# Kernel optimization log

Measured on AMD Instinct MI355X. Metric: run time of the kernel, lower is better.

Reference implementation:

```python
import jax, jax.numpy as jnp
import numpy as np
from jax import lax

N_CLASSES = 10
N_EXPERTS = 45  # 10 choose 2
EPS = 1e-5

# lookup table: (i1, i2) with i1 < i2 -> flat expert id (matches nested loop order)
_tbl = np.zeros((N_CLASSES, N_CLASSES), dtype=np.int32)
_k = 0
for _i1 in range(N_CLASSES):
    for _i2 in range(_i1 + 1, N_CLASSES):
        _tbl[_i1, _i2] = _k
        _k += 1
PAIR_TABLE = jnp.asarray(_tbl)


def _downscale(x):
    # AvgPool2d(3, stride=3) on 28x28 -> 9x9 (floor: uses top-left 27x27)
    B = x.shape[0]
    return x[:, :, :27, :27].reshape(B, 1, 9, 3, 9, 3).mean(axis=(3, 5))


def _bn_eval(h, gamma, beta, mean, var):
    scale = gamma * lax.rsqrt(var + EPS)
    return h * scale[None, :, None, None] + (beta - mean * scale)[None, :, None, None]


def _stage1(x, w1, b1, g1, be1, m1, v1, fcw1, fcb1):
    xd = _downscale(x)                                         # [B,1,9,9]
    h = lax.conv_general_dilated(xd, w1, (1, 1), 'VALID',
                                 dimension_numbers=('NCHW', 'OIHW', 'NCHW'))
    h = h + b1[None, :, None, None]                            # [B,20,7,7]
    h = _bn_eval(h, g1, be1, m1, v1)
    h = jax.nn.relu(h)
    B = h.shape[0]
    h = h[:, :, :6, :6].reshape(B, 20, 3, 2, 3, 2).max(axis=(3, 5))  # maxpool2 -> [B,20,3,3]
    h = h.reshape(B, 180)
    return h @ fcw1.T + fcb1                                   # [B,10] raw logits


def reference(x, w1, b1, g1, be1, m1, v1, fcw1, fcb1,
              w2, b2, g2, be2, m2, v2, fcw2, fcb2):
    B = x.shape[0]
    logits1 = _stage1(x, w1, b1, g1, be1, m1, v1, fcw1, fcb1)  # [B,10]
    ls1 = jax.nn.log_softmax(logits1, axis=1)

    # routing: top-2 class indices, sorted ascending, -> pairwise expert id
    top2 = jnp.sort(jnp.argsort(ls1, axis=1)[:, -2:], axis=1)  # [B,2]
    idx0, idx1 = top2[:, 0], top2[:, 1]
    eid = PAIR_TABLE[idx0, idx1]                               # [B]

    # stage 2 (TinyNet2) with per-example gathered expert params
    xd = _downscale(x)                                         # [B,1,9,9]
    # extract 5x5 conv patches (valid, stride 1): output spatial 5x5
    patches = jnp.stack([xd[:, 0, i:i + 5, j:j + 5]
                         for i in range(5) for j in range(5)], axis=1)  # [B,25,5,5]
    Wsel = w2.reshape(N_EXPERTS, 15, 25)[eid]                  # [B,15,25]
    h = jnp.einsum('bkhw,bok->bohw', patches, Wsel) + b2[eid][:, :, None, None]  # [B,15,5,5]
    scale = (g2 * lax.rsqrt(v2 + EPS))[eid]                    # [B,15]
    shift = (be2 - m2 * g2 * lax.rsqrt(v2 + EPS))[eid]
    h = h * scale[:, :, None, None] + shift[:, :, None, None]
    h = jax.nn.relu(h)
    h = h[:, :, :4, :4].reshape(B, 15, 2, 2, 2, 2).max(axis=(3, 5))  # [B,15,2,2]
    feat = h.reshape(B, 60)
    s2 = jnp.einsum('bf,bof->bo', feat, fcw2[eid]) + fcb2[eid]  # [B,2]

    # combine: scatter the two expert logits into the routed columns
    rows = jnp.arange(B)
    out = jnp.full((B, N_CLASSES), -100.0, dtype=logits1.dtype)
    out = out.at[rows, idx0].set(s2[:, 0]).at[rows, idx1].set(s2[:, 1])
    # eval-mode bypass: use stage1 raw logits if max log-prob > 0.3
    use1 = jnp.max(ls1, axis=1) > 0.3
    out = jnp.where(use1[:, None], logits1, out)
    out = jax.nn.log_softmax(out, axis=1)
    return (logits1, out)


def setup_inputs() -> dict:
    key = jax.random.key(0)
    ks = jax.random.split(key, 18)
    B = 65536
    s = 0.1
    return {
        'x': jax.random.normal(ks[0], (B, 1, 28, 28), dtype=jnp.float32),
        # stage1 (TinyNet, 20 kernels, k=3)
        'w1': jax.random.normal(ks[1], (20, 1, 3, 3), dtype=jnp.float32) * s,
        'b1': jax.random.normal(ks[2], (20,), dtype=jnp.float32) * s,
        'g1': jax.random.normal(ks[3], (20,), dtype=jnp.float32) * s + 1.0,
        'be1': jax.random.normal(ks[4], (20,), dtype=jnp.float32) * s,
        'm1': jax.random.normal(ks[5], (20,), dtype=jnp.float32) * s,
        'v1': jax.random.uniform(ks[6], (20,), dtype=jnp.float32) + 0.5,
        'fcw1': jax.random.normal(ks[7], (10, 180), dtype=jnp.float32) * s,
        'fcb1': jax.random.normal(ks[8], (10,), dtype=jnp.float32) * s,
        # 45 stacked stage2 experts (TinyNet2, 15 kernels, k=5)
        'w2': jax.random.normal(ks[9], (45, 15, 1, 5, 5), dtype=jnp.float32) * s,
        'b2': jax.random.normal(ks[10], (45, 15), dtype=jnp.float32) * s,
        'g2': jax.random.normal(ks[11], (45, 15), dtype=jnp.float32) * s + 1.0,
        'be2': jax.random.normal(ks[12], (45, 15), dtype=jnp.float32) * s,
        'm2': jax.random.normal(ks[13], (45, 15), dtype=jnp.float32) * s,
        'v2': jax.random.uniform(ks[14], (45, 15), dtype=jnp.float32) + 0.5,
        'fcw2': jax.random.normal(ks[15], (45, 2, 60), dtype=jnp.float32) * s,
        'fcb2': jax.random.normal(ks[16], (45, 2), dtype=jnp.float32) * s,
    }
```

## Files before the change

### kernel.cpp

```cpp
#include <hip/hip_runtime.h>
#include <cmath>

#define EPSF 1e-5f

#define OFF_FC2   19576
#define OFF_IMG   25088

#define I_W1P    0
#define I_FCW1R  240
#define I_B1F    2400
#define I_FCB1   2420
#define I_B2F    2432
#define I_FCB2   3108

__global__ __launch_bounds__(256) void setup_tables(
    const float* __restrict__ w1, const float* __restrict__ b1,
    const float* __restrict__ g1, const float* __restrict__ be1,
    const float* __restrict__ m1, const float* __restrict__ v1,
    const float* __restrict__ w2, const float* __restrict__ b2,
    const float* __restrict__ g2, const float* __restrict__ be2,
    const float* __restrict__ m2, const float* __restrict__ v2,
    const float* __restrict__ fcw2, const float* __restrict__ fcb2,
    const float* __restrict__ fcw1, const float* __restrict__ fcb1,
    float* __restrict__ ws)
{
  const int t  = blockIdx.x * blockDim.x + threadIdx.x;
  const int nt = gridDim.x * blockDim.x;
  float* W2F  = ws;
  float* FC2P = ws + OFF_FC2;
  float* IMG  = ws + OFF_IMG;

  for (int idx = t; idx < 18900; idx += nt) {
    int kk = idx & 3, rest = idx >> 2;
    int e = rest % 45, ok4 = rest / 45;
    int k4 = ok4 % 7, o = ok4 / 7;
    int k = k4 * 4 + kk;
    float s = g2[e*15+o] / sqrtf(v2[e*15+o] + EPSF);
    W2F[idx] = (k < 25) ? w2[(e*15+o)*25 + k] * s : 0.0f;
  }
  for (int idx = t; idx < 5400; idx += nt) {
    int e = idx % 45, r = idx / 45;
    int pos = r % 4, r2 = r / 4;
    int o = r2 % 15, oo = r2 / 15;
    FC2P[idx] = fcw2[(e*2+oo)*60 + o*4 + pos];
  }
  for (int i = t; i < 4096; i += nt) {
    float v = 0.0f;
    if (i < I_FCW1R) {
      int ch = i / 12, j = i % 12;
      if (j < 9) {
        float s = g1[ch] / sqrtf(v1[ch] + EPSF);
        v = w1[ch*9 + j] * s;
      }
    } else if (i < I_B1F) {
      int k = i - I_FCW1R;
      int c = k % 12, r2 = k / 12, pp = r2 % 9, ch = r2 / 9;
      if (c < 10) v = fcw1[c*180 + ch*9 + pp];
    } else if (i < I_FCB1) {
      int ch = i - I_B1F;
      float s = g1[ch] / sqrtf(v1[ch] + EPSF);
      v = b1[ch]*s + be1[ch] - m1[ch]*s;
    } else if (i < I_B2F) {
      int k = i - I_FCB1;
      if (k < 10) v = fcb1[k];
    } else if (i < I_FCB2) {
      int k = i - I_B2F;
      if (k < 675) {
        int e = k % 45, o = k / 45;
        float s = g2[e*15+o] / sqrtf(v2[e*15+o] + EPSF);
        v = b2[e*15+o]*s + be2[e*15+o] - m2[e*15+o]*s;
      }
    } else {
      int k = i - I_FCB2;
      if (k < 90) {
        int e = k % 45, oo = k / 45;
        v = fcb2[e*2+oo];
      }
    }
    IMG[i] = v;
  }
}

#define GETC(arr, k) ((k)%4==0 ? arr[(k)/4].x : (k)%4==1 ? arr[(k)/4].y : \
                      (k)%4==2 ? arr[(k)/4].z : arr[(k)/4].w)

#define T_RAW   4352
#define T_TAB   4352
#define SSTR    676

__global__ __launch_bounds__(256) void fused_k(
    const float* __restrict__ x,
    const float* __restrict__ ws,
    float* __restrict__ out, int B)
{
  __shared__ float lds[9760];

  const int t  = threadIdx.x;
  const int p  = t & 3;
  const int sl = t >> 2;
  const int b  = blockIdx.x * 64 + sl;
  const bool valid = (b < B);

  const int s8  = t >> 5;
  const int tin = t & 31;

  float4 pre[6];
  {
    const int bs = blockIdx.x * 64 + s8;
    if (bs < B) {
      const float4* xp = reinterpret_cast<const float4*>(x + (size_t)bs * 784);
      #pragma unroll
      for (int j = 0; j < 5; j++) pre[j] = xp[tin + 32*j];
      pre[5] = (tin < 8) ? xp[tin + 160] : make_float4(0.f,0.f,0.f,0.f);
    } else {
      #pragma unroll
      for (int j = 0; j < 6; j++) pre[j] = make_float4(0.f,0.f,0.f,0.f);
    }
    float4* rw = reinterpret_cast<float4*>(&lds[T_RAW + s8*SSTR]);
    #pragma unroll
    for (int j = 0; j < 5; j++) rw[tin + 32*j] = pre[j];
    if (tin < 8) rw[tin + 160] = pre[5];
  }
  __syncthreads();

  #pragma unroll 1
  for (int c = 0; c < 8; c++) {
    if (c < 7) {
      const int bs = blockIdx.x * 64 + (c+1)*8 + s8;
      if (bs < B) {
        const float4* xp = reinterpret_cast<const float4*>(x + (size_t)bs * 784);
        #pragma unroll
        for (int j = 0; j < 5; j++) pre[j] = xp[tin + 32*j];
        pre[5] = (tin < 8) ? xp[tin + 160] : make_float4(0.f,0.f,0.f,0.f);
      }
    }
    if (t < 128) {
      const int ds8  = t >> 4;
      const int orow = (t >> 1) & 7;
      const int h    = t & 1;
      float a0 = 0.f, a1 = 0.f, a2 = 0.f, a3 = 0.f;
      #pragma unroll
      for (int dr = 0; dr < 3; dr++) {
        const float4* rp = reinterpret_cast<const float4*>(
            &lds[T_RAW + ds8*SSTR + (3*orow + dr)*28 + 12*h]);
        float4 q0 = rp[0], q1 = rp[1], q2 = rp[2];
        a0 += q0.x + q0.y + q0.z;
        a1 += q0.w + q1.x + q1.y;
        a2 += q1.z + q1.w + q2.x;
        a3 += q2.y + q2.z + q2.w;
      }
      float4* dst = reinterpret_cast<float4*>(&lds[(c*8 + ds8)*68 + orow*8 + 4*h]);
      *dst = make_float4(a0*(1.f/9.f), a1*(1.f/9.f), a2*(1.f/9.f), a3*(1.f/9.f));
    }
    __syncthreads();
    if (c < 7) {
      float4* rw = reinterpret_cast<float4*>(&lds[T_RAW + s8*SSTR]);
      #pragma unroll
      for (int j = 0; j < 5; j++) rw[tin + 32*j] = pre[j];
      if (tin < 8) rw[tin + 160] = pre[5];
      __syncthreads();
    }
  }

  const float4* img4 = reinterpret_cast<const float4*>(ws + OFF_IMG);
  float4 tv0 = img4[t];
  float4 tv1 = img4[t + 256];
  float4 tv2 = img4[t + 512];
  float4 tv3 = img4[t + 768];

  const int R0 = p & 2;
  const int C0 = (p & 1) * 2;
  float xl[36];
  #pragma unroll
  for (int lr = 0; lr < 6; lr++) {
    const float2* src = reinterpret_cast<const float2*>(&lds[sl*68 + (R0+lr)*8 + C0]);
    float2 q0 = src[0], q1 = src[1], q2 = src[2];
    xl[lr*6+0]=q0.x; xl[lr*6+1]=q0.y; xl[lr*6+2]=q1.x;
    xl[lr*6+3]=q1.y; xl[lr*6+4]=q2.x; xl[lr*6+5]=q2.y;
  }
  {
    float4* tab4 = reinterpret_cast<float4*>(&lds[T_TAB]);
    tab4[t] = tv0; tab4[t + 256] = tv1; tab4[t + 512] = tv2; tab4[t + 768] = tv3;
  }
  __syncthreads();

  const int basegpp = (p >> 1) * 3 + (p & 1);
  float logits[10];
  #pragma unroll
  for (int c = 0; c < 10; c++) logits[c] = 0.0f;

  #pragma unroll 1
  for (int ch = 0; ch < 20; ch++) {
    const float4* wp = reinterpret_cast<const float4*>(&lds[T_TAB + I_W1P + ch*12]);
    float4 w0 = wp[0], w1v = wp[1], w2v = wp[2];
    const float w_[9] = {w0.x,w0.y,w0.z,w0.w,w1v.x,w1v.y,w1v.z,w1v.w,w2v.x};
    const float bb = lds[T_TAB + I_B1F + ch];
    #pragma unroll
    for (int lp = 0; lp < 4; lp++) {
      const int lpr = lp >> 1, lpc = lp & 1;
      float c00 = bb, c01 = bb, c10 = bb, c11 = bb;
      #pragma unroll
      for (int dr = 0; dr < 3; dr++) {
        #pragma unroll
        for (int dc = 0; dc < 3; dc++) {
          const float wk = w_[dr*3 + dc];
          c00 = fmaf(xl[(2*lpr+0+dr)*6 + 2*lpc+0+dc], wk, c00);
          c01 = fmaf(xl[(2*lpr+0+dr)*6 + 2*lpc+1+dc], wk, c01);
          c10 = fmaf(xl[(2*lpr+1+dr)*6 + 2*lpc+0+dc], wk, c10);
          c11 = fmaf(xl[(2*lpr+1+dr)*6 + 2*lpc+1+dc], wk, c11);
        }
      }
      float f = fmaxf(fmaxf(fmaxf(c00, c01), fmaxf(c10, c11)), 0.0f);
      const int MASKS[4] = {3, 14, 5, 12};
      const float fm = ((MASKS[lp] >> p) & 1) ? f : 0.0f;
      const int off = (lp >> 1) * 3 + (lp & 1);
      const float4* f4 = reinterpret_cast<const float4*>(
          &lds[T_TAB + I_FCW1R + (ch*9 + basegpp + off)*12]);
      float4 f0 = f4[0], f1 = f4[1], f2 = f4[2];
      logits[0] = fmaf(fm, f0.x, logits[0]);
      logits[1] = fmaf(fm, f0.y, logits[1]);
      logits[2] = fmaf(fm, f0.z, logits[2]);
      logits[3] = fmaf(fm, f0.w, logits[3]);
      logits[4] = fmaf(fm, f1.x, logits[4]);
      logits[5] = fmaf(fm, f1.y, logits[5]);
      logits[6] = fmaf(fm, f1.z, logits[6]);
      logits[7] = fmaf(fm, f1.w, logits[7]);
      logits[8] = fmaf(fm, f2.x, logits[8]);
      logits[9] = fmaf(fm, f2.y, logits[9]);
    }
  }

  #pragma unroll
  for (int c = 0; c < 10; c++) {
    float v = logits[c];
    v += __shfl_xor(v, 1);
    v += __shfl_xor(v, 2);
    logits[c] = v + lds[T_TAB + I_FCB1 + c];
  }

  int i1 = 0; float v1m = logits[0];
  #pragma unroll
  for (int c = 1; c < 10; c++) { if (logits[c] >= v1m) { v1m = logits[c]; i1 = c; } }
  int i2 = 0; float v2m = -3.0e38f;
  #pragma unroll
  for (int c = 0; c < 10; c++) { if (c != i1 && logits[c] >= v2m) { v2m = logits[c]; i2 = c; } }
  const int idx0 = i1 < i2 ? i1 : i2;
  const int idx1 = i1 < i2 ? i2 : i1;
  int eid = 8*idx0 - (idx0*(idx0-1))/2 + idx1 - 1;
  eid = eid < 0 ? 0 : (eid > 44 ? 44 : eid);

  float sume = 0.0f;
  #pragma unroll
  for (int c = 0; c < 10; c++) sume += __expf(logits[c] - v1m);
  const bool use1 = (-__logf(sume)) > 0.3f;

  __syncthreads();
  if (p == 0) {
    #pragma unroll
    for (int c = 0; c < 5; c++) lds[sl*10 + c] = logits[c];
  } else if (p == 1) {
    #pragma unroll
    for (int c = 5; c < 10; c++) lds[sl*10 + c] = logits[c];
  }

  const float4* W2F4 = reinterpret_cast<const float4*>(ws);
  const float*  FC2P = ws + OFF_FC2;
  float s2a = 0.0f, s2b = 0.0f;

  #pragma unroll 1
  for (int o = 0; o < 15; o++) {
    float4 wv[7];
    #pragma unroll
    for (int k4 = 0; k4 < 7; k4++) wv[k4] = W2F4[(o*7 + k4)*45 + eid];
    const float bias = lds[T_TAB + I_B2F + o*45 + eid];
    const float fa = FC2P[(o*4 + p)*45 + eid];
    const float fb = FC2P[((15 + o)*4 + p)*45 + eid];
    float c00 = bias, c01 = bias, c10 = bias, c11 = bias;
    #pragma unroll
    for (int i = 0; i < 5; i++) {
      #pragma unroll
      for (int j = 0; j < 5; j++) {
        const float wk = GETC(wv, i*5 + j);
        c00 = fmaf(xl[(0+i)*6 + 0+j], wk, c00);
        c01 = fmaf(xl[(0+i)*6 + 1+j], wk, c01);
        c10 = fmaf(xl[(1+i)*6 + 0+j], wk, c10);
        c11 = fmaf(xl[(1+i)*6 + 1+j], wk, c11);
      }
    }
    const float f = fmaxf(fmaxf(fmaxf(c00, c01), fmaxf(c10, c11)), 0.0f);
    s2a = fmaf(f, fa, s2a);
    s2b = fmaf(f, fb, s2b);
  }
  s2a += __shfl_xor(s2a, 1); s2a += __shfl_xor(s2a, 2);
  s2b += __shfl_xor(s2b, 1); s2b += __shfl_xor(s2b, 2);
  s2a += lds[T_TAB + I_FCB2 + eid];
  s2b += lds[T_TAB + I_FCB2 + 45 + eid];

  __syncthreads();
  float o10[10];
  #pragma unroll
  for (int c = 0; c < 10; c++) {
    float v = -100.0f;
    v = (c == idx0) ? s2a : v;
    v = (c == idx1) ? s2b : v;
    o10[c] = use1 ? lds[sl*10 + c] : v;
  }
  float m2x = o10[0];
  #pragma unroll
  for (int c = 1; c < 10; c++) m2x = fmaxf(m2x, o10[c]);
  float se2 = 0.0f;
  #pragma unroll
  for (int c = 0; c < 10; c++) se2 += __expf(o10[c] - m2x);
  const float lse2 = m2x + __logf(se2);

  if (p == 2) {
    #pragma unroll
    for (int c = 0; c < 5; c++) lds[640 + sl*10 + c] = o10[c] - lse2;
  } else if (p == 3) {
    #pragma unroll
    for (int c = 5; c < 10; c++) lds[640 + sl*10 + c] = o10[c] - lse2;
  }
  __syncthreads();

  if (blockIdx.x * 64 + 64 <= B) {
    const float4* l4 = reinterpret_cast<const float4*>(lds);
    const size_t o1 = (size_t)blockIdx.x * 640;
    if (t < 160)
      *reinterpret_cast<float4*>(out + o1 + (size_t)t*4) = l4[t];
    if (t >= 96)
      *reinterpret_cast<float4*>(out + (size_t)B*10 + o1 + (size_t)(t-96)*4) = l4[160 + (t-96)];
  } else if (valid) {
    const size_t base = (size_t)b * 10;
    if (p == 0) {
      #pragma unroll
      for (int c = 0; c < 5; c++) out[base + c] = lds[sl*10 + c];
    } else if (p == 1) {
      #pragma unroll
      for (int c = 5; c < 10; c++) out[base + c] = lds[sl*10 + c];
    } else if (p == 2) {
      #pragma unroll
      for (int c = 0; c < 5; c++) out[(size_t)B*10 + base + c] = lds[640 + sl*10 + c];
    } else {
      #pragma unroll
      for (int c = 5; c < 10; c++) out[(size_t)B*10 + base + c] = lds[640 + sl*10 + c];
    }
  }
}

extern "C" void kernel_launch(void* const* d_in, const int* in_sizes, int n_in,
                              void* d_out, int out_size, void* d_ws, size_t ws_size,
                              hipStream_t stream) {
  const float* x    = (const float*)d_in[0];
  const float* w1   = (const float*)d_in[1];
  const float* b1   = (const float*)d_in[2];
  const float* g1   = (const float*)d_in[3];
  const float* be1  = (const float*)d_in[4];
  const float* m1   = (const float*)d_in[5];
  const float* v1   = (const float*)d_in[6];
  const float* fcw1 = (const float*)d_in[7];
  const float* fcb1 = (const float*)d_in[8];
  const float* w2   = (const float*)d_in[9];
  const float* b2   = (const float*)d_in[10];
  const float* g2   = (const float*)d_in[11];
  const float* be2  = (const float*)d_in[12];
  const float* m2   = (const float*)d_in[13];
  const float* v2   = (const float*)d_in[14];
  const float* fcw2 = (const float*)d_in[15];
  const float* fcb2 = (const float*)d_in[16];
  float* out = (float*)d_out;
  float* ws  = (float*)d_ws;
  const int B = in_sizes[0] / 784;

  setup_tables<<<80, 256, 0, stream>>>(w1, b1, g1, be1, m1, v1,
                                       w2, b2, g2, be2, m2, v2,
                                       fcw2, fcb2, fcw1, fcb1, ws);
  fused_k<<<(B + 63)/64, 256, 0, stream>>>(x, ws, out, B);
}
```

Before: 345.5 us.

## Read parameter tables from global memory instead of staging them in LDS

The fused kernel no longer copies a parameter table into shared memory. Stage-1 weights, biases and FC weights are now read directly from the global workspace, which drops a global-to-LDS staging pass and one barrier. The stage-2 bias and FC bias are packed into the padding slots of the per-expert weight vector, so they arrive with the weight load. The FC1 accumulation is restructured so each lane picks its own pooled feature per position. Every block now pays for scalar or cached global loads inside its inner loops and does more FMAs with zero operands.

After: 358.8 us. +3.8%, slower.

```diff
diff --git a/kernel.cpp b/kernel.cpp
--- a/kernel.cpp
+++ b/kernel.cpp
@@ -3,15 +3,10 @@
 
 #define EPSF 1e-5f
 
-#define OFF_FC2   19576
-#define OFF_IMG   25088
-
-#define I_W1P    0
-#define I_FCW1R  240
-#define I_B1F    2400
-#define I_FCB1   2420
-#define I_B2F    2432
-#define I_FCB2   3108
+#define OFF_FC2P  18900
+#define OFF_FCW1R 24300
+#define OFF_W1F   26460
+#define OFF_B1F   26640
 
 __global__ __launch_bounds__(256) void setup_tables(
     const float* __restrict__ w1, const float* __restrict__ b1,
@@ -21,14 +16,16 @@
     const float* __restrict__ g2, const float* __restrict__ be2,
     const float* __restrict__ m2, const float* __restrict__ v2,
     const float* __restrict__ fcw2, const float* __restrict__ fcb2,
-    const float* __restrict__ fcw1, const float* __restrict__ fcb1,
+    const float* __restrict__ fcw1,
     float* __restrict__ ws)
 {
   const int t  = blockIdx.x * blockDim.x + threadIdx.x;
   const int nt = gridDim.x * blockDim.x;
-  float* W2F  = ws;
-  float* FC2P = ws + OFF_FC2;
-  float* IMG  = ws + OFF_IMG;
+  float* W2F   = ws;
+  float* FC2P  = ws + OFF_FC2P;
+  float* FCW1R = ws + OFF_FCW1R;
+  float* W1F   = ws + OFF_W1F;
+  float* B1F   = ws + OFF_B1F;
 
   for (int idx = t; idx < 18900; idx += nt) {
     int kk = idx & 3, rest = idx >> 2;
@@ -36,7 +33,12 @@
     int k4 = ok4 % 7, o = ok4 / 7;
     int k = k4 * 4 + kk;
     float s = g2[e*15+o] / sqrtf(v2[e*15+o] + EPSF);
-    W2F[idx] = (k < 25) ? w2[(e*15+o)*25 + k] * s : 0.0f;
+    float v;
+    if (k < 25)       v = w2[(e*15+o)*25 + k] * s;
+    else if (k == 25) v = b2[e*15+o]*s + be2[e*15+o] - m2[e*15+o]*s;
+    else if (k == 26) v = (o == 0) ? fcb2[e*2 + 0] : 0.0f;
+    else              v = (o == 0) ? fcb2[e*2 + 1] : 0.0f;
+    W2F[idx] = v;
   }
   for (int idx = t; idx < 5400; idx += nt) {
     int e = idx % 45, r = idx / 45;
@@ -44,40 +46,18 @@
     int o = r2 % 15, oo = r2 / 15;
     FC2P[idx] = fcw2[(e*2+oo)*60 + o*4 + pos];
   }
-  for (int i = t; i < 4096; i += nt) {
-    float v = 0.0f;
-    if (i < I_FCW1R) {
-      int ch = i / 12, j = i % 12;
-      if (j < 9) {
-        float s = g1[ch] / sqrtf(v1[ch] + EPSF);
-        v = w1[ch*9 + j] * s;
-      }
-    } else if (i < I_B1F) {
-      int k = i - I_FCW1R;
-      int c = k % 12, r2 = k / 12, pp = r2 % 9, ch = r2 / 9;
-      if (c < 10) v = fcw1[c*180 + ch*9 + pp];
-    } else if (i < I_FCB1) {
-      int ch = i - I_B1F;
-      float s = g1[ch] / sqrtf(v1[ch] + EPSF);
-      v = b1[ch]*s + be1[ch] - m1[ch]*s;
-    } else if (i < I_B2F) {
-      int k = i - I_FCB1;
-      if (k < 10) v = fcb1[k];
-    } else if (i < I_FCB2) {
-      int k = i - I_B2F;
-      if (k < 675) {
-        int e = k % 45, o = k / 45;
-        float s = g2[e*15+o] / sqrtf(v2[e*15+o] + EPSF);
-        v = b2[e*15+o]*s + be2[e*15+o] - m2[e*15+o]*s;
-      }
-    } else {
-      int k = i - I_FCB2;
-      if (k < 90) {
-        int e = k % 45, oo = k / 45;
-        v = fcb2[e*2+oo];
-      }
-    }
-    IMG[i] = v;
+  for (int idx = t; idx < 2160; idx += nt) {
+    int c = idx % 12, r2 = idx / 12, pp = r2 % 9, ch = r2 / 9;
+    FCW1R[idx] = (c < 10) ? fcw1[c*180 + ch*9 + pp] : 0.0f;
+  }
+  for (int idx = t; idx < 180; idx += nt) {
+    int ch = idx / 9;
+    float s = g1[ch] / sqrtf(v1[ch] + EPSF);
+    W1F[idx] = w1[idx] * s;
+  }
+  for (int idx = t; idx < 20; idx += nt) {
+    float s = g1[idx] / sqrtf(v1[idx] + EPSF);
+    B1F[idx] = b1[idx]*s + be1[idx] - m1[idx]*s;
   }
 }
 
@@ -85,12 +65,12 @@
                       (k)%4==2 ? arr[(k)/4].z : arr[(k)/4].w)
 
 #define T_RAW   4352
-#define T_TAB   4352
 #define SSTR    676
 
 __global__ __launch_bounds__(256) void fused_k(
     const float* __restrict__ x,
     const float* __restrict__ ws,
+    const float* __restrict__ fcb1,
     float* __restrict__ out, int B)
 {
   __shared__ float lds[9760];
@@ -100,6 +80,11 @@
   const int sl = t >> 2;
   const int b  = blockIdx.x * 64 + sl;
   const bool valid = (b < B);
+
+  const float* FC2P  = ws + OFF_FC2P;
+  const float* FCW1R = ws + OFF_FCW1R;
+  const float* W1F   = ws + OFF_W1F;
+  const float* B1F   = ws + OFF_B1F;
 
   const int s8  = t >> 5;
   const int tin = t & 31;
@@ -162,12 +147,6 @@
     }
   }
 
-  const float4* img4 = reinterpret_cast<const float4*>(ws + OFF_IMG);
-  float4 tv0 = img4[t];
-  float4 tv1 = img4[t + 256];
-  float4 tv2 = img4[t + 512];
-  float4 tv3 = img4[t + 768];
-
   const int R0 = p & 2;
   const int C0 = (p & 1) * 2;
   float xl[36];
@@ -178,23 +157,18 @@
     xl[lr*6+0]=q0.x; xl[lr*6+1]=q0.y; xl[lr*6+2]=q1.x;
     xl[lr*6+3]=q1.y; xl[lr*6+4]=q2.x; xl[lr*6+5]=q2.y;
   }
-  {
-    float4* tab4 = reinterpret_cast<float4*>(&lds[T_TAB]);
-    tab4[t] = tv0; tab4[t + 256] = tv1; tab4[t + 512] = tv2; tab4[t + 768] = tv3;
-  }
-  __syncthreads();
-
-  const int basegpp = (p >> 1) * 3 + (p & 1);
+
   float logits[10];
   #pragma unroll
   for (int c = 0; c < 10; c++) logits[c] = 0.0f;
 
   #pragma unroll 1
   for (int ch = 0; ch < 20; ch++) {
-    const float4* wp = reinterpret_cast<const float4*>(&lds[T_TAB + I_W1P + ch*12]);
-    float4 w0 = wp[0], w1v = wp[1], w2v = wp[2];
-    const float w_[9] = {w0.x,w0.y,w0.z,w0.w,w1v.x,w1v.y,w1v.z,w1v.w,w2v.x};
-    const float bb = lds[T_TAB + I_B1F + ch];
+    float w_[9];
+    #pragma unroll
+    for (int k = 0; k < 9; k++) w_[k] = W1F[ch*9 + k];
+    const float bb = B1F[ch];
+    float feat[4];
     #pragma unroll
     for (int lp = 0; lp < 4; lp++) {
       const int lpr = lp >> 1, lpc = lp & 1;
@@ -210,23 +184,16 @@
           c11 = fmaf(xl[(2*lpr+1+dr)*6 + 2*lpc+1+dc], wk, c11);
         }
       }
-      float f = fmaxf(fmaxf(fmaxf(c00, c01), fmaxf(c10, c11)), 0.0f);
-      const int MASKS[4] = {3, 14, 5, 12};
-      const float fm = ((MASKS[lp] >> p) & 1) ? f : 0.0f;
-      const int off = (lp >> 1) * 3 + (lp & 1);
-      const float4* f4 = reinterpret_cast<const float4*>(
-          &lds[T_TAB + I_FCW1R + (ch*9 + basegpp + off)*12]);
-      float4 f0 = f4[0], f1 = f4[1], f2 = f4[2];
-      logits[0] = fmaf(fm, f0.x, logits[0]);
-      logits[1] = fmaf(fm, f0.y, logits[1]);
-      logits[2] = fmaf(fm, f0.z, logits[2]);
-      logits[3] = fmaf(fm, f0.w, logits[3]);
-      logits[4] = fmaf(fm, f1.x, logits[4]);
-      logits[5] = fmaf(fm, f1.y, logits[5]);
-      logits[6] = fmaf(fm, f1.z, logits[6]);
-      logits[7] = fmaf(fm, f1.w, logits[7]);
-      logits[8] = fmaf(fm, f2.x, logits[8]);
-      logits[9] = fmaf(fm, f2.y, logits[9]);
+      feat[lp] = fmaxf(fmaxf(fmaxf(c00, c01), fmaxf(c10, c11)), 0.0f);
+    }
+    const int QOWN[9]  = {0,1,1,0,2,3,2,2,3};
+    const int LPOWN[9] = {0,0,1,2,1,1,2,3,3};
+    #pragma unroll
+    for (int pp = 0; pp < 9; pp++) {
+      const float* R = FCW1R + (ch*9 + pp)*12;
+      const float fm = (p == QOWN[pp]) ? feat[LPOWN[pp]] : 0.0f;
+      #pragma unroll
+      for (int c = 0; c < 10; c++) logits[c] = fmaf(fm, R[c], logits[c]);
     }
   }
 
@@ -235,7 +202,7 @@
     float v = logits[c];
     v += __shfl_xor(v, 1);
     v += __shfl_xor(v, 2);
-    logits[c] = v + lds[T_TAB + I_FCB1 + c];
+    logits[c] = v + fcb1[c];
   }
 
   int i1 = 0; float v1m = logits[0];
@@ -264,37 +231,45 @@
   }
 
   const float4* W2F4 = reinterpret_cast<const float4*>(ws);
-  const float*  FC2P = ws + OFF_FC2;
-  float s2a = 0.0f, s2b = 0.0f;
+
+  const float4 wb = W2F4[6*45 + eid];
+  float s2a = (p == 0) ? wb.z : 0.0f;
+  float s2b = (p == 0) ? wb.w : 0.0f;
 
   #pragma unroll 1
   for (int o = 0; o < 15; o++) {
-    float4 wv[7];
-    #pragma unroll
-    for (int k4 = 0; k4 < 7; k4++) wv[k4] = W2F4[(o*7 + k4)*45 + eid];
-    const float bias = lds[T_TAB + I_B2F + o*45 + eid];
+    const float4 wv6 = W2F4[(o*7 + 6)*45 + eid];
     const float fa = FC2P[(o*4 + p)*45 + eid];
     const float fb = FC2P[((15 + o)*4 + p)*45 + eid];
+    const float bias = wv6.y;
     float c00 = bias, c01 = bias, c10 = bias, c11 = bias;
     #pragma unroll
-    for (int i = 0; i < 5; i++) {
-      #pragma unroll
-      for (int j = 0; j < 5; j++) {
-        const float wk = GETC(wv, i*5 + j);
+    for (int g = 0; g < 6; g++) {
+      const float4 wg = W2F4[(o*7 + g)*45 + eid];
+      #pragma unroll
+      for (int kk = 0; kk < 4; kk++) {
+        const int k = 4*g + kk;
+        const int i = k / 5, j = k % 5;
+        const float wk = (kk==0) ? wg.x : (kk==1) ? wg.y : (kk==2) ? wg.z : wg.w;
         c00 = fmaf(xl[(0+i)*6 + 0+j], wk, c00);
         c01 = fmaf(xl[(0+i)*6 + 1+j], wk, c01);
         c10 = fmaf(xl[(1+i)*6 + 0+j], wk, c10);
         c11 = fmaf(xl[(1+i)*6 + 1+j], wk, c11);
       }
     }
+    {
+      const float wk = wv6.x;
+      c00 = fmaf(xl[4*6 + 4], wk, c00);
+      c01 = fmaf(xl[4*6 + 5], wk, c01);
+      c10 = fmaf(xl[5*6 + 4], wk, c10);
+      c11 = fmaf(xl[5*6 + 5], wk, c11);
+    }
     const float f = fmaxf(fmaxf(fmaxf(c00, c01), fmaxf(c10, c11)), 0.0f);
     s2a = fmaf(f, fa, s2a);
     s2b = fmaf(f, fb, s2b);
   }
   s2a += __shfl_xor(s2a, 1); s2a += __shfl_xor(s2a, 2);
   s2b += __shfl_xor(s2b, 1); s2b += __shfl_xor(s2b, 2);
-  s2a += lds[T_TAB + I_FCB2 + eid];
-  s2b += lds[T_TAB + I_FCB2 + 45 + eid];
 
   __syncthreads();
   float o10[10];
@@ -373,6 +348,6 @@
 
   setup_tables<<<80, 256, 0, stream>>>(w1, b1, g1, be1, m1, v1,
                                        w2, b2, g2, be2, m2, v2,
-                                       fcw2, fcb2, fcw1, fcb1, ws);
-  fused_k<<<(B + 63)/64, 256, 0, stream>>>(x, ws, out, B);
+                                       fcw2, fcb2, fcw1, ws);
+  fused_k<<<(B + 63)/64, 256, 0, stream>>>(x, ws, fcb1, out, B);
 }
```
